# Kernel optimization log

Hardware: AMD Instinct MI355X
Metric: run time of the kernel (lower is better)

## Reference

```python
import jax, jax.numpy as jnp
import numpy as np

MARGIN = 5.0
NUM_CLASSES = 21


def setup_inputs() -> dict:
    key = jax.random.key(0)
    k1, k2, k3 = jax.random.split(key, 3)
    B, D, C = 65536, 512, NUM_CLASSES
    features = jax.random.normal(k1, (B, D), dtype=jnp.float32)
    centers = jax.random.normal(k2, (C, D), dtype=jnp.float32)
    labels = jax.random.randint(k3, (B,), 0, C, dtype=jnp.int64)
    return {"features": features, "centers": centers, "labels": labels}


def reference(features, centers, labels):
    # Halved squared euclidean distances, batch x num_classes, via the
    # ||f||^2 + ||c||^2 - 2 f.c expansion (avoids a B x C x D intermediate).
    f2 = jnp.sum(features * features, axis=1, keepdims=True)      # (B, 1)
    c2 = jnp.sum(centers * centers, axis=1)[None, :]              # (1, C)
    d = 0.5 * (f2 + c2 - 2.0 * (features @ centers.T))            # (B, C)

    B = features.shape[0]
    pos = d[jnp.arange(B), labels]                                 # dist to own center
    same = labels[:, None] == jnp.arange(NUM_CLASSES)[None, :]     # (B, C)
    neg = jnp.min(jnp.where(same, jnp.inf, d), axis=1)             # nearest other center
    loss = jnp.mean(jax.nn.relu(pos + MARGIN - neg))
    return loss
```

## Files before the change

### kernel.cpp

```cpp
#include <hip/hip_runtime.h>
#include <float.h>

#define DIM      512
#define NCLS     21
#define MARGIN_V 5.0f
#define ROWS_PB  64
#define NWAVES   8
#define DSLICE   (DIM / NWAVES)
#define DC       16
#define NSTAGE   (DSLICE / DC)
#define LPAD     (DC + 1)
#define TILEF    (ROWS_PB * LPAD)
#define CST      (NCLS + 1)

__global__ __launch_bounds__(64)
void center_norm_kernel(const float* __restrict__ centers,
                        float* __restrict__ halfc2) {
    const int c = blockIdx.x;
    const int t = threadIdx.x;
    float s = 0.f;
#pragma unroll
    for (int i = 0; i < DIM / 64; ++i) {
        float v = centers[c * DIM + i * 64 + t];
        s = fmaf(v, v, s);
    }
#pragma unroll
    for (int off = 32; off > 0; off >>= 1)
        s += __shfl_down(s, off, 64);
    if (t == 0) halfc2[c] = 0.5f * s;
}

__global__ __launch_bounds__(512, 8)
void tcl_main_kernel(const float* __restrict__ feat,
                     const float* __restrict__ centers,
                     const int* __restrict__ labels,
                     const float* __restrict__ halfc2,
                     float* __restrict__ out) {
    __shared__ float lds[NWAVES * TILEF];

    const int tid  = threadIdx.x;
    const int w    = __builtin_amdgcn_readfirstlane(tid >> 6);
    const int t    = tid & 63;
    const int row0 = blockIdx.x * ROWS_PB;

    float* mytile = &lds[w * TILEF];

    float acc[NCLS];
#pragma unroll
    for (int c = 0; c < NCLS; ++c) acc[c] = 0.f;

    const float4* fbase = reinterpret_cast<const float4*>(feat);
    const int rsub = t >> 2;
    const int j4   = t & 3;
    const size_t gbase = (size_t)(row0 + rsub) * (DIM / 4)
                       + (size_t)w * (DSLICE / 4) + j4;

    float4 pre[4];
#pragma unroll
    for (int i = 0; i < 4; ++i)
        pre[i] = fbase[gbase + (size_t)i * 16 * (DIM / 4)];

    const int wbase = rsub * LPAD + j4 * 4;

#pragma unroll 1
    for (int s = 0; s < NSTAGE; ++s) {
#pragma unroll
        for (int i = 0; i < 4; ++i) {
            int b = i * 16 * LPAD + wbase;
            mytile[b + 0] = pre[i].x;
            mytile[b + 1] = pre[i].y;
            mytile[b + 2] = pre[i].z;
            mytile[b + 3] = pre[i].w;
        }
        if (s + 1 < NSTAGE) {
#pragma unroll
            for (int i = 0; i < 4; ++i)
                pre[i] = fbase[gbase + (size_t)i * 16 * (DIM / 4)
                               + (size_t)(s + 1) * (DC / 4)];
        }
        const int dbase = w * DSLICE + s * DC;
#pragma unroll 2
        for (int jj = 0; jj < DC; jj += 4) {
            float f0 = mytile[t * LPAD + jj + 0];
            float f1 = mytile[t * LPAD + jj + 1];
            float f2 = mytile[t * LPAD + jj + 2];
            float f3 = mytile[t * LPAD + jj + 3];
#pragma unroll
            for (int c = 0; c < NCLS; ++c) {
                const float* cp = &centers[c * DIM + dbase + jj];
                acc[c] = fmaf(f0, cp[0],
                          fmaf(f1, cp[1],
                           fmaf(f2, cp[2],
                            fmaf(f3, cp[3], acc[c]))));
            }
        }
    }

    float* comb = lds;
    __syncthreads();
    if (w >= 4) {
        float* p = &comb[((w - 4) * ROWS_PB + t) * CST];
#pragma unroll
        for (int c = 0; c < NCLS; ++c) p[c] = acc[c];
    }
    __syncthreads();
    if (w < 4) {
        const float* p = &comb[(w * ROWS_PB + t) * CST];
#pragma unroll
        for (int c = 0; c < NCLS; ++c) acc[c] += p[c];
    }
    __syncthreads();
    if (w == 2 || w == 3) {
        float* p = &comb[((w - 2) * ROWS_PB + t) * CST];
#pragma unroll
        for (int c = 0; c < NCLS; ++c) p[c] = acc[c];
    }
    __syncthreads();
    if (w < 2) {
        const float* p = &comb[(w * ROWS_PB + t) * CST];
#pragma unroll
        for (int c = 0; c < NCLS; ++c) acc[c] += p[c];
    }
    __syncthreads();
    if (w == 1) {
        float* p = &comb[t * CST];
#pragma unroll
        for (int c = 0; c < NCLS; ++c) p[c] = acc[c];
    }
    __syncthreads();
    if (w == 0) {
        const float* p = &comb[t * CST];
        const int lab = labels[row0 + t];
        float pos = 0.f, neg = FLT_MAX;
#pragma unroll
        for (int c = 0; c < NCLS; ++c) {
            float e = halfc2[c] - (acc[c] + p[c]);
            pos = (c == lab) ? e : pos;
            neg = (c == lab) ? neg : fminf(neg, e);
        }
        float v = fmaxf(pos + MARGIN_V - neg, 0.f);
#pragma unroll
        for (int off = 32; off > 0; off >>= 1)
            v += __shfl_down(v, off, 64);
        if (t == 0) atomicAdd(out, v * (1.0f / 65536.f));
    }
}

extern "C" void kernel_launch(void* const* d_in, const int* in_sizes, int n_in,
                              void* d_out, int out_size, void* d_ws, size_t ws_size,
                              hipStream_t stream) {
    const float* feat    = (const float*)d_in[0];
    const float* centers = (const float*)d_in[1];
    const int*   labels  = (const int*)d_in[2];
    float* out    = (float*)d_out;
    float* halfc2 = (float*)d_ws;

    hipMemsetAsync(d_out, 0, (size_t)out_size * sizeof(float), stream);
    center_norm_kernel<<<NCLS, 64, 0, stream>>>(centers, halfc2);

    const int nblocks = 65536 / ROWS_PB;
    tcl_main_kernel<<<nblocks, 512, 0, stream>>>(feat, centers, labels, halfc2, out);
}
```

Baseline: 209.0 us.

## Load feature slices directly into registers, dropping LDS staging pipeline

Each lane now loads its own row's 64-float slice as 16 float4 loads straight into registers, removing the staged LDS transpose and prefetch loop. The dot products then run per class over the register-held values. Labels are loaded early, and launch bounds drop to one block per SM, which allows more registers. The trade-off is that the per-lane loads become strided across rows (each lane reads a 256-byte chunk of a different row), so coalescing is worse. The higher register use may also lower occupancy and hurt latency hiding.

New measurement: 210.7 us. No clear change (+0.8%).

```diff
diff --git a/kernel.cpp b/kernel.cpp
--- a/kernel.cpp
+++ b/kernel.cpp
@@ -4,14 +4,11 @@
 #define DIM      512
 #define NCLS     21
 #define MARGIN_V 5.0f
-#define ROWS_PB  64
 #define NWAVES   8
 #define DSLICE   (DIM / NWAVES)
-#define DC       16
-#define NSTAGE   (DSLICE / DC)
-#define LPAD     (DC + 1)
-#define TILEF    (ROWS_PB * LPAD)
-#define CST      (NCLS + 1)
+#define ROWS_PB  64
+#define SST      (NCLS + 1)
+#define LDSF     (4 * 64 * SST)
 
 __global__ __launch_bounds__(64)
 void center_norm_kernel(const float* __restrict__ centers,
@@ -30,107 +27,80 @@
     if (t == 0) halfc2[c] = 0.5f * s;
 }
 
-__global__ __launch_bounds__(512, 8)
+__global__ __launch_bounds__(512, 1)
 void tcl_main_kernel(const float* __restrict__ feat,
                      const float* __restrict__ centers,
                      const int* __restrict__ labels,
                      const float* __restrict__ halfc2,
                      float* __restrict__ out) {
-    __shared__ float lds[NWAVES * TILEF];
+    __shared__ float scratch[LDSF];
 
     const int tid  = threadIdx.x;
     const int w    = __builtin_amdgcn_readfirstlane(tid >> 6);
     const int t    = tid & 63;
     const int row0 = blockIdx.x * ROWS_PB;
 
-    float* mytile = &lds[w * TILEF];
+    int lab = 0;
+    if (w == 0) lab = labels[row0 + t];
 
     float acc[NCLS];
 #pragma unroll
     for (int c = 0; c < NCLS; ++c) acc[c] = 0.f;
 
-    const float4* fbase = reinterpret_cast<const float4*>(feat);
-    const int rsub = t >> 2;
-    const int j4   = t & 3;
-    const size_t gbase = (size_t)(row0 + rsub) * (DIM / 4)
-                       + (size_t)w * (DSLICE / 4) + j4;
+    const float4* f4p = reinterpret_cast<const float4*>(feat);
+    const size_t  rb  = (size_t)(row0 + t) * (DIM / 4) + (size_t)w * (DSLICE / 4);
+    float4 fv[16];
+#pragma unroll
+    for (int j = 0; j < 16; ++j) fv[j] = f4p[rb + j];
 
-    float4 pre[4];
+    const int dbase = w * DSLICE;
 #pragma unroll
-    for (int i = 0; i < 4; ++i)
-        pre[i] = fbase[gbase + (size_t)i * 16 * (DIM / 4)];
-
-    const int wbase = rsub * LPAD + j4 * 4;
-
-#pragma unroll 1
-    for (int s = 0; s < NSTAGE; ++s) {
+    for (int c = 0; c < NCLS; ++c) {
+        const float* __restrict__ cp = &centers[c * DIM + dbase];
+        float a = acc[c];
 #pragma unroll
-        for (int i = 0; i < 4; ++i) {
-            int b = i * 16 * LPAD + wbase;
-            mytile[b + 0] = pre[i].x;
-            mytile[b + 1] = pre[i].y;
-            mytile[b + 2] = pre[i].z;
-            mytile[b + 3] = pre[i].w;
+        for (int j = 0; j < 16; ++j) {
+            a = fmaf(fv[j].x, cp[4 * j + 0],
+                 fmaf(fv[j].y, cp[4 * j + 1],
+                  fmaf(fv[j].z, cp[4 * j + 2],
+                   fmaf(fv[j].w, cp[4 * j + 3], a))));
         }
-        if (s + 1 < NSTAGE) {
-#pragma unroll
-            for (int i = 0; i < 4; ++i)
-                pre[i] = fbase[gbase + (size_t)i * 16 * (DIM / 4)
-                               + (size_t)(s + 1) * (DC / 4)];
-        }
-        const int dbase = w * DSLICE + s * DC;
-#pragma unroll 2
-        for (int jj = 0; jj < DC; jj += 4) {
-            float f0 = mytile[t * LPAD + jj + 0];
-            float f1 = mytile[t * LPAD + jj + 1];
-            float f2 = mytile[t * LPAD + jj + 2];
-            float f3 = mytile[t * LPAD + jj + 3];
-#pragma unroll
-            for (int c = 0; c < NCLS; ++c) {
-                const float* cp = &centers[c * DIM + dbase + jj];
-                acc[c] = fmaf(f0, cp[0],
-                          fmaf(f1, cp[1],
-                           fmaf(f2, cp[2],
-                            fmaf(f3, cp[3], acc[c]))));
-            }
-        }
+        acc[c] = a;
     }
 
-    float* comb = lds;
     __syncthreads();
     if (w >= 4) {
-        float* p = &comb[((w - 4) * ROWS_PB + t) * CST];
+        float* p = &scratch[((w - 4) * 64 + t) * SST];
 #pragma unroll
         for (int c = 0; c < NCLS; ++c) p[c] = acc[c];
     }
     __syncthreads();
     if (w < 4) {
-        const float* p = &comb[(w * ROWS_PB + t) * CST];
+        const float* p = &scratch[(w * 64 + t) * SST];
 #pragma unroll
         for (int c = 0; c < NCLS; ++c) acc[c] += p[c];
     }
     __syncthreads();
     if (w == 2 || w == 3) {
-        float* p = &comb[((w - 2) * ROWS_PB + t) * CST];
+        float* p = &scratch[((w - 2) * 64 + t) * SST];
 #pragma unroll
         for (int c = 0; c < NCLS; ++c) p[c] = acc[c];
     }
     __syncthreads();
     if (w < 2) {
-        const float* p = &comb[(w * ROWS_PB + t) * CST];
+        const float* p = &scratch[(w * 64 + t) * SST];
 #pragma unroll
         for (int c = 0; c < NCLS; ++c) acc[c] += p[c];
     }
     __syncthreads();
     if (w == 1) {
-        float* p = &comb[t * CST];
+        float* p = &scratch[t * SST];
 #pragma unroll
         for (int c = 0; c < NCLS; ++c) p[c] = acc[c];
     }
     __syncthreads();
     if (w == 0) {
-        const float* p = &comb[t * CST];
-        const int lab = labels[row0 + t];
+        const float* p = &scratch[t * SST];
         float pos = 0.f, neg = FLT_MAX;
 #pragma unroll
         for (int c = 0; c < NCLS; ++c) {
```
